# Performance work log

Hardware: AMD Instinct MI355X
Metric: run time of the kernel (lower is better)

Reference implementation:

```python
import jax, jax.numpy as jnp
import numpy as np

B, CIN, H, W = 16, 3, 128, 128
C = 256          # out_channels
NH = 8           # num_heads
HD = C // NH     # head_dim = 32
SCALE = HD ** -0.5
EPS = 1e-5


def setup_inputs() -> dict:
    key = jax.random.key(0)
    ks = jax.random.split(key, 8)
    def xavier(k, fan_out, fan_in):
        lim = np.sqrt(6.0 / (fan_in + fan_out))
        return jax.random.uniform(k, (fan_out, fan_in), jnp.float32, -lim, lim)
    return {
        "x": jax.random.normal(ks[0], (B, CIN, H, W), jnp.float32),
        "Wi": xavier(ks[1], C, CIN),      # input_conv 1x1
        "bi": jnp.zeros((C,), jnp.float32),
        "Wqkv": xavier(ks[2], 3 * C, C),  # qkv_conv 1x1, no bias
        "Wo": xavier(ks[3], C, C),        # output_proj
        "bo": jnp.zeros((C,), jnp.float32),
        "Wf": xavier(ks[4], C, C),        # feature_update_conv
        "bf": jnp.zeros((C,), jnp.float32),
        "gamma": jnp.ones((C,), jnp.float32),
        "beta": jnp.zeros((C,), jnp.float32),
        "rmean": jnp.zeros((C,), jnp.float32),
        "rvar": jnp.ones((C,), jnp.float32),
    }


def reference(x, Wi, bi, Wqkv, Wo, bo, Wf, bf, gamma, beta, rmean, rvar):
    b, _, h, w = x.shape
    hw = h * w
    # input 1x1 conv
    x1 = jnp.einsum('oi,bihw->bohw', Wi, x) + bi[:, None, None]
    # qkv 1x1 conv, reshape (b, NH, 3, HD, h*w) matching torch channel layout
    qkv = jnp.einsum('oi,bihw->bohw', Wqkv, x1).reshape(b, NH, 3, HD, hw)
    q, k, v = qkv[:, :, 0], qkv[:, :, 1], qkv[:, :, 2]  # each (b, NH, HD, hw)
    # channel-channel attention: (b, NH, HD, HD), sigmoid gate (no softmax)
    attention = jax.nn.sigmoid(jnp.einsum('bndp,bnep->bnde', q, k) * SCALE)
    A = jnp.einsum('bnde,bnep->bndp', attention, v).reshape(b, C, h, w)
    A = jnp.einsum('oi,bihw->bohw', Wo, A) + bo[:, None, None]
    A = jnp.einsum('oi,bihw->bohw', Wf, A) + bf[:, None, None]
    # BatchNorm2d (eval mode: running stats)
    inv = gamma / jnp.sqrt(rvar + EPS)
    A = (A - rmean[:, None, None]) * inv[:, None, None] + beta[:, None, None]
    A = jax.nn.silu(A)  # dropout is identity in eval
    out = A + x1
    return (out, attention)
```

## Files before the change

kernel.cpp:

```cpp
#include <hip/hip_runtime.h>
#include <math.h>


#define HW 16384
#define NBATCH 16
static constexpr float SCALE_ = 0.17677669529663687f;
static constexpr float EPS_ = 1e-5f;

typedef float f32x4 __attribute__((ext_vector_type(4)));

#define WS_PART 0
#define WS_WFO  4096
#define WS_BFO  69632
#define WS_WB4  69888
#define WS_AQ   71168
#define WS_A4G  75776

__device__ __forceinline__ float sigmoidf_(float z) {
  return __builtin_amdgcn_rcpf(1.0f + __expf(-z));
}

__global__ __launch_bounds__(256) void k_prep(
    const float* __restrict__ x,
    const float* __restrict__ Wi, const float* __restrict__ bi,
    const float* __restrict__ Wqkv,
    const float* __restrict__ Wo, const float* __restrict__ bo,
    const float* __restrict__ Wf, const float* __restrict__ bf,
    float* __restrict__ part, float* __restrict__ Wfo,
    float* __restrict__ bfo, float* __restrict__ Wb4,
    float* __restrict__ aqg)
{
  const int bx = blockIdx.x;
  const int tid = threadIdx.x;
  if (bx < 256) {
    const int b = bx >> 4;
    const int pi = bx & 15;
    const int p0 = pi * 1024 + tid * 4;
    const float4 a0 = *reinterpret_cast<const float4*>(x + (size_t)(b * 3 + 0) * HW + p0);
    const float4 a1 = *reinterpret_cast<const float4*>(x + (size_t)(b * 3 + 1) * HW + p0);
    const float4 a2 = *reinterpret_cast<const float4*>(x + (size_t)(b * 3 + 2) * HW + p0);
    float v[9];
    v[0] = a0.x * a0.x + a0.y * a0.y + a0.z * a0.z + a0.w * a0.w;
    v[1] = a0.x * a1.x + a0.y * a1.y + a0.z * a1.z + a0.w * a1.w;
    v[2] = a0.x * a2.x + a0.y * a2.y + a0.z * a2.z + a0.w * a2.w;
    v[3] = a1.x * a1.x + a1.y * a1.y + a1.z * a1.z + a1.w * a1.w;
    v[4] = a1.x * a2.x + a1.y * a2.y + a1.z * a2.z + a1.w * a2.w;
    v[5] = a2.x * a2.x + a2.y * a2.y + a2.z * a2.z + a2.w * a2.w;
    v[6] = a0.x + a0.y + a0.z + a0.w;
    v[7] = a1.x + a1.y + a1.z + a1.w;
    v[8] = a2.x + a2.y + a2.z + a2.w;
    __shared__ float wred[4][9];
    const int lane = tid & 63, wid = tid >> 6;
#pragma unroll
    for (int k = 0; k < 9; ++k) {
      float s = v[k];
#pragma unroll
      for (int off = 32; off; off >>= 1) s += __shfl_down(s, off, 64);
      if (lane == 0) wred[wid][k] = s;
    }
    __syncthreads();
    if (tid < 9) {
      part[bx * 9 + tid] = wred[0][tid] + wred[1][tid] + wred[2][tid] + wred[3][tid];
    }
  } else if (bx < 512) {
    const int o = bx - 256;
    const float* wfr = Wf + (size_t)o * 256;
    const int i = tid;
    float acc = 0.f;
#pragma unroll 32
    for (int k = 0; k < 256; ++k) acc = fmaf(wfr[k], Wo[(size_t)k * 256 + i], acc);
    Wfo[(size_t)o * 256 + i] = acc;
  } else if (bx == 512) {
    Wb4[tid * 4 + 0] = Wi[tid * 3 + 0];
    Wb4[tid * 4 + 1] = Wi[tid * 3 + 1];
    Wb4[tid * 4 + 2] = Wi[tid * 3 + 2];
    Wb4[tid * 4 + 3] = bi[tid];
    float acc = bf[tid];
    const float* wfr = Wf + (size_t)tid * 256;
#pragma unroll 16
    for (int k = 0; k < 256; ++k) acc = fmaf(wfr[k], bo[k], acc);
    bfo[tid] = acc;
  } else {
    const int blk = bx - 513;
    const int rl = tid >> 2;
    const int ch = tid & 3;
    const int row = blk * 64 + rl;
    const float* wr = Wqkv + (size_t)row * 256 + ch * 64;
    float c0 = 0, c1 = 0, c2 = 0, c3 = 0;
#pragma unroll 8
    for (int c = 0; c < 64; ++c) {
      const float w = wr[c];
      const int cc = ch * 64 + c;
      c0 = fmaf(w, Wi[cc * 3 + 0], c0);
      c1 = fmaf(w, Wi[cc * 3 + 1], c1);
      c2 = fmaf(w, Wi[cc * 3 + 2], c2);
      c3 = fmaf(w, bi[cc], c3);
    }
    __shared__ float red[64][4][4];
    red[rl][ch][0] = c0; red[rl][ch][1] = c1;
    red[rl][ch][2] = c2; red[rl][ch][3] = c3;
    __syncthreads();
    const int j = tid & 3;
    aqg[(size_t)(blk * 64 + rl) * 4 + j] =
        red[rl][0][j] + red[rl][1][j] + red[rl][2][j] + red[rl][3][j];
  }
}

__global__ __launch_bounds__(256) void k_solveA(
    const float* __restrict__ part, const float* __restrict__ aqg,
    float* __restrict__ att_out,
    float* __restrict__ A4g)
{
  const int n = blockIdx.x;
  const int b = blockIdx.y;
  const int tid = threadIdx.x;
  __shared__ float Ms[9];
  __shared__ float aqh[96][5];
  __shared__ float att_s[32][33];
  if (tid < 9) {
    float s = 0.f;
    for (int j = 0; j < 16; ++j) s += part[(b * 16 + j) * 9 + tid];
    Ms[tid] = s;
  }
  if (tid < 96) {
    const float4 v = *reinterpret_cast<const float4*>(aqg + (size_t)(n * 96 + tid) * 4);
    aqh[tid][0] = v.x; aqh[tid][1] = v.y; aqh[tid][2] = v.z; aqh[tid][3] = v.w;
  }
  __syncthreads();
  const float M00 = Ms[0], M01 = Ms[1], M02 = Ms[2], M11 = Ms[3], M12 = Ms[4], M22 = Ms[5];
  const float s0 = Ms[6], s1 = Ms[7], s2 = Ms[8];
#pragma unroll
  for (int r = 0; r < 4; ++r) {
    const int idx = tid + r * 256;
    const int d = idx >> 5, e = idx & 31;
    const float* q = aqh[d];
    const float* k = aqh[32 + e];
    const float q0 = q[0], q1 = q[1], q2 = q[2], q3 = q[3];
    const float k0 = k[0], k1 = k[1], k2 = k[2], k3 = k[3];
    const float t = q0 * (M00 * k0 + M01 * k1 + M02 * k2)
                  + q1 * (M01 * k0 + M11 * k1 + M12 * k2)
                  + q2 * (M02 * k0 + M12 * k1 + M22 * k2)
                  + q3 * (s0 * k0 + s1 * k1 + s2 * k2)
                  + k3 * (s0 * q0 + s1 * q1 + s2 * q2)
                  + 16384.0f * q3 * k3;
    const float a = sigmoidf_(SCALE_ * t);
    att_s[d][e] = a;
    att_out[(size_t)(b * 8 + n) * 1024 + idx] = a;
  }
  __syncthreads();
  if (tid < 128) {
    const int d = tid >> 2, j = tid & 3;
    float acc = 0.f;
#pragma unroll 8
    for (int e = 0; e < 32; ++e) acc = fmaf(att_s[d][e], aqh[64 + e][j], acc);
    A4g[(size_t)(b * 256 + n * 32 + d) * 4 + j] = acc;
  }
}

__global__ __launch_bounds__(256) void k_final(
    const float* __restrict__ x,
    const float* __restrict__ Wfo, const float* __restrict__ bfo,
    const float* __restrict__ A4g, const float4* __restrict__ Wb4,
    const float* __restrict__ gamma, const float* __restrict__ beta,
    const float* __restrict__ rmean, const float* __restrict__ rvar,
    float* __restrict__ out)
{
  const int b = blockIdx.z;
  const int c0 = blockIdx.y * 32;
  const int tid = threadIdx.x;
  __shared__ float4 A4v[256];
  __shared__ float Wfo_s[32][257];
  __shared__ float4 partial[32][9];
  __shared__ float4 sg[32], sw[32];

  A4v[tid] = *reinterpret_cast<const float4*>(A4g + ((size_t)b * 256 + tid) * 4);
#pragma unroll
  for (int it = 0; it < 8; ++it) {
    const int idx = tid + it * 256;
    const int r = idx >> 6, kq = idx & 63;
    const float4 v = *reinterpret_cast<const float4*>(
        Wfo + ((size_t)(c0 + r) * 256 + kq * 4));
    Wfo_s[r][kq * 4 + 0] = v.x; Wfo_s[r][kq * 4 + 1] = v.y;
    Wfo_s[r][kq * 4 + 2] = v.z; Wfo_s[r][kq * 4 + 3] = v.w;
  }
  __syncthreads();
  {
    const int ks = tid >> 5, o = tid & 31;
    float4 acc = make_float4(0.f, 0.f, 0.f, 0.f);
#pragma unroll 8
    for (int i = 0; i < 32; ++i) {
      const float w = Wfo_s[o][ks * 32 + i];
      const float4 a = A4v[ks * 32 + i];
      acc.x = fmaf(w, a.x, acc.x); acc.y = fmaf(w, a.y, acc.y);
      acc.z = fmaf(w, a.z, acc.z); acc.w = fmaf(w, a.w, acc.w);
    }
    partial[o][ks] = acc;
  }
  __syncthreads();
  if (tid < 32) {
    const int o = tid;
    float4 s = partial[o][0];
#pragma unroll
    for (int k2 = 1; k2 < 8; ++k2) {
      const float4 p = partial[o][k2];
      s.x += p.x; s.y += p.y; s.z += p.z; s.w += p.w;
    }
    const int c = c0 + o;
    const float inv = gamma[c] / sqrtf(rvar[c] + EPS_);
    const float g3 = (s.w + bfo[c] - rmean[c]) * inv + beta[c];
    sg[o] = make_float4(s.x * inv, s.y * inv, s.z * inv, g3);
    sw[o] = Wb4[c];
  }
  __syncthreads();

  const int pbase = blockIdx.x * 4096 + tid * 4;
  const float* xb = x + (size_t)b * 3 * HW;
  float4 X0[4], X1[4], X2[4];
#pragma unroll
  for (int pi = 0; pi < 4; ++pi) {
    const int p = pbase + pi * 1024;
    X0[pi] = *reinterpret_cast<const float4*>(xb + p);
    X1[pi] = *reinterpret_cast<const float4*>(xb + HW + p);
    X2[pi] = *reinterpret_cast<const float4*>(xb + 2 * HW + p);
  }
  float* ob = out + (size_t)(b * 256 + c0) * HW;
  for (int ci = 0; ci < 32; ++ci) {
    const float4 g = sg[ci];
    const float4 w = sw[ci];
    float* oc = ob + (size_t)ci * HW + pbase;
#pragma unroll
    for (int pi = 0; pi < 4; ++pi) {
      const float4 A = X0[pi], B = X1[pi], C = X2[pi];
      f32x4 r;
      {
        const float y = fmaf(g.x, A.x, fmaf(g.y, B.x, fmaf(g.z, C.x, g.w)));
        r.x = y * sigmoidf_(y) + fmaf(w.x, A.x, fmaf(w.y, B.x, fmaf(w.z, C.x, w.w)));
      }
      {
        const float y = fmaf(g.x, A.y, fmaf(g.y, B.y, fmaf(g.z, C.y, g.w)));
        r.y = y * sigmoidf_(y) + fmaf(w.x, A.y, fmaf(w.y, B.y, fmaf(w.z, C.y, w.w)));
      }
      {
        const float y = fmaf(g.x, A.z, fmaf(g.y, B.z, fmaf(g.z, C.z, g.w)));
        r.z = y * sigmoidf_(y) + fmaf(w.x, A.z, fmaf(w.y, B.z, fmaf(w.z, C.z, w.w)));
      }
      {
        const float y = fmaf(g.x, A.w, fmaf(g.y, B.w, fmaf(g.z, C.w, g.w)));
        r.w = y * sigmoidf_(y) + fmaf(w.x, A.w, fmaf(w.y, B.w, fmaf(w.z, C.w, w.w)));
      }
      *reinterpret_cast<f32x4*>(oc + pi * 1024) = r;
    }
  }
}

extern "C" void kernel_launch(void* const* d_in, const int* in_sizes, int n_in,
                              void* d_out, int out_size, void* d_ws, size_t ws_size,
                              hipStream_t stream) {
  const float* x     = (const float*)d_in[0];
  const float* Wi    = (const float*)d_in[1];
  const float* bi    = (const float*)d_in[2];
  const float* Wqkv  = (const float*)d_in[3];
  const float* Wo    = (const float*)d_in[4];
  const float* bo    = (const float*)d_in[5];
  const float* Wf    = (const float*)d_in[6];
  const float* bf    = (const float*)d_in[7];
  const float* gamma = (const float*)d_in[8];
  const float* beta  = (const float*)d_in[9];
  const float* rmean = (const float*)d_in[10];
  const float* rvar  = (const float*)d_in[11];

  float* out = (float*)d_out;
  float* att = out + (size_t)NBATCH * 256 * HW;
  float* wsf = (float*)d_ws;

  k_prep<<<dim3(525), dim3(256), 0, stream>>>(x, Wi, bi, Wqkv, Wo, bo, Wf, bf,
                                              wsf + WS_PART, wsf + WS_WFO,
                                              wsf + WS_BFO, wsf + WS_WB4,
                                              wsf + WS_AQ);
  k_solveA<<<dim3(8, NBATCH), dim3(256), 0, stream>>>(wsf + WS_PART, wsf + WS_AQ,
                                                      att, wsf + WS_A4G);
  k_final<<<dim3(4, 8, NBATCH), dim3(256), 0, stream>>>(
      x, wsf + WS_WFO, wsf + WS_BFO, wsf + WS_A4G,
      (const float4*)(wsf + WS_WB4), gamma, beta, rmean, rvar, out);
}
```

Before: 64.96 us.

## Fuse attention solve into final kernel, recomputing per block to drop a launch

Removes the separate k_solveA kernel and has every k_final block recompute the sigmoid attention and the attention-times-V product for all 8 heads of its batch into shared memory. Only one block per batch writes the attention output. This drops a kernel launch and the global round trip of the A4 intermediate. In exchange it adds redundant compute in each of 32 blocks per batch, extra barriers, and more shared memory per block, which may lower occupancy.

```diff
diff --git a/kernel.cpp b/kernel.cpp
--- a/kernel.cpp
+++ b/kernel.cpp
@@ -14,7 +14,6 @@
 #define WS_BFO  69632
 #define WS_WB4  69888
 #define WS_AQ   71168
-#define WS_A4G  75776
 
 __device__ __forceinline__ float sigmoidf_(float z) {
   return __builtin_amdgcn_rcpf(1.0f + __expf(-z));
@@ -106,74 +105,27 @@
   }
 }
 
-__global__ __launch_bounds__(256) void k_solveA(
-    const float* __restrict__ part, const float* __restrict__ aqg,
-    float* __restrict__ att_out,
-    float* __restrict__ A4g)
-{
-  const int n = blockIdx.x;
-  const int b = blockIdx.y;
-  const int tid = threadIdx.x;
-  __shared__ float Ms[9];
-  __shared__ float aqh[96][5];
-  __shared__ float att_s[32][33];
-  if (tid < 9) {
-    float s = 0.f;
-    for (int j = 0; j < 16; ++j) s += part[(b * 16 + j) * 9 + tid];
-    Ms[tid] = s;
-  }
-  if (tid < 96) {
-    const float4 v = *reinterpret_cast<const float4*>(aqg + (size_t)(n * 96 + tid) * 4);
-    aqh[tid][0] = v.x; aqh[tid][1] = v.y; aqh[tid][2] = v.z; aqh[tid][3] = v.w;
-  }
-  __syncthreads();
-  const float M00 = Ms[0], M01 = Ms[1], M02 = Ms[2], M11 = Ms[3], M12 = Ms[4], M22 = Ms[5];
-  const float s0 = Ms[6], s1 = Ms[7], s2 = Ms[8];
-#pragma unroll
-  for (int r = 0; r < 4; ++r) {
-    const int idx = tid + r * 256;
-    const int d = idx >> 5, e = idx & 31;
-    const float* q = aqh[d];
-    const float* k = aqh[32 + e];
-    const float q0 = q[0], q1 = q[1], q2 = q[2], q3 = q[3];
-    const float k0 = k[0], k1 = k[1], k2 = k[2], k3 = k[3];
-    const float t = q0 * (M00 * k0 + M01 * k1 + M02 * k2)
-                  + q1 * (M01 * k0 + M11 * k1 + M12 * k2)
-                  + q2 * (M02 * k0 + M12 * k1 + M22 * k2)
-                  + q3 * (s0 * k0 + s1 * k1 + s2 * k2)
-                  + k3 * (s0 * q0 + s1 * q1 + s2 * q2)
-                  + 16384.0f * q3 * k3;
-    const float a = sigmoidf_(SCALE_ * t);
-    att_s[d][e] = a;
-    att_out[(size_t)(b * 8 + n) * 1024 + idx] = a;
-  }
-  __syncthreads();
-  if (tid < 128) {
-    const int d = tid >> 2, j = tid & 3;
-    float acc = 0.f;
-#pragma unroll 8
-    for (int e = 0; e < 32; ++e) acc = fmaf(att_s[d][e], aqh[64 + e][j], acc);
-    A4g[(size_t)(b * 256 + n * 32 + d) * 4 + j] = acc;
-  }
-}
-
 __global__ __launch_bounds__(256) void k_final(
     const float* __restrict__ x,
     const float* __restrict__ Wfo, const float* __restrict__ bfo,
-    const float* __restrict__ A4g, const float4* __restrict__ Wb4,
+    const float* __restrict__ aqg, const float* __restrict__ part,
+    const float4* __restrict__ Wb4,
     const float* __restrict__ gamma, const float* __restrict__ beta,
     const float* __restrict__ rmean, const float* __restrict__ rvar,
-    float* __restrict__ out)
+    float* __restrict__ att_out, float* __restrict__ out)
 {
   const int b = blockIdx.z;
   const int c0 = blockIdx.y * 32;
   const int tid = threadIdx.x;
-  __shared__ float4 A4v[256];
+  const bool writer = (blockIdx.x == 0) && (blockIdx.y == 0);
+  __shared__ float Ms[9];
+  __shared__ float aqh[96][5];
+  __shared__ float att_s[32][33];
+  __shared__ float A4vf[256][4];
   __shared__ float Wfo_s[32][257];
   __shared__ float4 partial[32][9];
   __shared__ float4 sg[32], sw[32];
 
-  A4v[tid] = *reinterpret_cast<const float4*>(A4g + ((size_t)b * 256 + tid) * 4);
 #pragma unroll
   for (int it = 0; it < 8; ++it) {
     const int idx = tid + it * 256;
@@ -183,14 +135,57 @@
     Wfo_s[r][kq * 4 + 0] = v.x; Wfo_s[r][kq * 4 + 1] = v.y;
     Wfo_s[r][kq * 4 + 2] = v.z; Wfo_s[r][kq * 4 + 3] = v.w;
   }
+  if (tid < 9) {
+    float s = 0.f;
+    for (int j = 0; j < 16; ++j) s += part[(b * 16 + j) * 9 + tid];
+    Ms[tid] = s;
+  }
   __syncthreads();
+  const float M00 = Ms[0], M01 = Ms[1], M02 = Ms[2], M11 = Ms[3], M12 = Ms[4], M22 = Ms[5];
+  const float s0 = Ms[6], s1 = Ms[7], s2 = Ms[8];
+
+  for (int n = 0; n < 8; ++n) {
+    if (tid < 96) {
+      const float4 v = *reinterpret_cast<const float4*>(aqg + (size_t)(n * 96 + tid) * 4);
+      aqh[tid][0] = v.x; aqh[tid][1] = v.y; aqh[tid][2] = v.z; aqh[tid][3] = v.w;
+    }
+    __syncthreads();
+#pragma unroll
+    for (int r = 0; r < 4; ++r) {
+      const int idx = tid + r * 256;
+      const int d = idx >> 5, e = idx & 31;
+      const float* q = aqh[d];
+      const float* k = aqh[32 + e];
+      const float q0 = q[0], q1 = q[1], q2 = q[2], q3 = q[3];
+      const float k0 = k[0], k1 = k[1], k2 = k[2], k3 = k[3];
+      const float t = q0 * (M00 * k0 + M01 * k1 + M02 * k2)
+                    + q1 * (M01 * k0 + M11 * k1 + M12 * k2)
+                    + q2 * (M02 * k0 + M12 * k1 + M22 * k2)
+                    + q3 * (s0 * k0 + s1 * k1 + s2 * k2)
+                    + k3 * (s0 * q0 + s1 * q1 + s2 * q2)
+                    + 16384.0f * q3 * k3;
+      const float a = sigmoidf_(SCALE_ * t);
+      att_s[d][e] = a;
+      if (writer) att_out[(size_t)(b * 8 + n) * 1024 + idx] = a;
+    }
+    __syncthreads();
+    if (tid < 128) {
+      const int d = tid >> 2, j = tid & 3;
+      float acc = 0.f;
+#pragma unroll 8
+      for (int e = 0; e < 32; ++e) acc = fmaf(att_s[d][e], aqh[64 + e][j], acc);
+      A4vf[n * 32 + d][j] = acc;
+    }
+    __syncthreads();
+  }
+
   {
     const int ks = tid >> 5, o = tid & 31;
     float4 acc = make_float4(0.f, 0.f, 0.f, 0.f);
 #pragma unroll 8
     for (int i = 0; i < 32; ++i) {
       const float w = Wfo_s[o][ks * 32 + i];
-      const float4 a = A4v[ks * 32 + i];
+      const float4 a = *reinterpret_cast<const float4*>(A4vf[ks * 32 + i]);
       acc.x = fmaf(w, a.x, acc.x); acc.y = fmaf(w, a.y, acc.y);
       acc.z = fmaf(w, a.z, acc.z); acc.w = fmaf(w, a.w, acc.w);
     }
@@ -277,9 +272,7 @@
                                               wsf + WS_PART, wsf + WS_WFO,
                                               wsf + WS_BFO, wsf + WS_WB4,
                                               wsf + WS_AQ);
-  k_solveA<<<dim3(8, NBATCH), dim3(256), 0, stream>>>(wsf + WS_PART, wsf + WS_AQ,
-                                                      att, wsf + WS_A4G);
   k_final<<<dim3(4, 8, NBATCH), dim3(256), 0, stream>>>(
-      x, wsf + WS_WFO, wsf + WS_BFO, wsf + WS_A4G,
-      (const float4*)(wsf + WS_WB4), gamma, beta, rmean, rvar, out);
-}
+      x, wsf + WS_WFO, wsf + WS_BFO, wsf + WS_AQ, wsf + WS_PART,
+      (const float4*)(wsf + WS_WB4), gamma, beta, rmean, rvar, att, out);
+}
```

Result: slower. 70.70 us (+8.8%).
